# Kernel tuning notes

Measured on AMD Instinct MI355X. Metric: run time of the kernel, lower is better.

Reference implementation:

```python
import jax, jax.numpy as jnp
import numpy as np

EPS = 1e-5
DN = ('NCHW', 'OIHW', 'NCHW')


def _conv3x3(x, w):
    return jax.lax.conv_general_dilated(x, w, (1, 1), 'SAME', dimension_numbers=DN)


def _bn_relu(x, g, b):
    # eval-mode BN: running_mean=0, running_var=1
    scale = (g / jnp.sqrt(1.0 + EPS))[None, :, None, None]
    return jax.nn.relu(x * scale + b[None, :, None, None])


def _double_conv(x, w1, g1, b1, w2, g2, b2):
    x = _bn_relu(_conv3x3(x, w1), g1, b1)
    return _bn_relu(_conv3x3(x, w2), g2, b2)


def _up2x_bilinear_align(x):
    # bilinear, align_corners=True, scale_factor=2
    def interp(a, axis, n_in):
        n_out = 2 * n_in
        pos = jnp.arange(n_out, dtype=jnp.float32) * (n_in - 1) / (n_out - 1)
        lo = jnp.floor(pos).astype(jnp.int32)
        hi = jnp.minimum(lo + 1, n_in - 1)
        w = pos - lo.astype(jnp.float32)
        sh = [1, 1, 1, 1]
        sh[axis] = n_out
        w = w.reshape(sh)
        return jnp.take(a, lo, axis=axis) * (1.0 - w) + jnp.take(a, hi, axis=axis) * w
    B, C, H, W = x.shape
    return interp(interp(x, 2, H), 3, W)


def _lstm_dir(seq, Wih, Whh, bih, bhh, reverse):
    # seq: (N, T, C) -> (N, T, Hh); PyTorch gate order i,f,g,o
    Hh = Whh.shape[1]
    xg = jnp.einsum('ntc,gc->ntg', seq, Wih) + (bih + bhh)
    if reverse:
        xg = xg[:, ::-1]
    xg = jnp.swapaxes(xg, 0, 1)  # (T, N, 4H)
    N = seq.shape[0]
    h0 = jnp.zeros((N, Hh), seq.dtype)

    def step(carry, gx):
        h, c = carry
        g = gx + h @ Whh.T
        i, f, gg, o = jnp.split(g, 4, axis=-1)
        c = jax.nn.sigmoid(f) * c + jax.nn.sigmoid(i) * jnp.tanh(gg)
        h = jax.nn.sigmoid(o) * jnp.tanh(c)
        return (h, c), h

    _, hs = jax.lax.scan(step, (h0, h0), xg)
    hs = jnp.swapaxes(hs, 0, 1)  # (N, T, Hh)
    if reverse:
        hs = hs[:, ::-1]
    return hs


def _bilstm(seq, Wf, Uf, bif, bhf, Wb, Ub, bib, bhb):
    return jnp.concatenate([
        _lstm_dir(seq, Wf, Uf, bif, bhf, False),
        _lstm_dir(seq, Wb, Ub, bib, bhb, True),
    ], axis=-1)


def _site_rows(x, lstm):
    # batched version of per-row LSTM: each row is a sequence over W, features C
    B, C, H, W = x.shape
    s = jnp.transpose(x, (0, 2, 3, 1)).reshape(B * H, W, C)
    out = _bilstm(s, *lstm)  # (B*H, W, C) since 2*hidden == C
    return jnp.transpose(out.reshape(B, H, W, C), (0, 3, 1, 2))


def _site_cols(x, lstm):
    # each column is a sequence over H, features C
    B, C, H, W = x.shape
    s = jnp.transpose(x, (0, 3, 2, 1)).reshape(B * W, H, C)
    out = _bilstm(s, *lstm)
    return jnp.transpose(out.reshape(B, W, H, C), (0, 3, 2, 1))


def setup_inputs() -> dict:
    key = jax.random.key(0)
    ks = jax.random.split(key, 24)
    d = {}
    d['x1'] = jax.random.normal(ks[0], (8, 128, 32, 32), jnp.float32)
    d['x2'] = jax.random.normal(ks[1], (8, 128, 64, 64), jnp.float32)
    # bidirectional LSTM: input 256, hidden 128
    d['lstm_Wih_f'] = jax.random.normal(ks[2], (512, 256), jnp.float32) * 0.06
    d['lstm_Whh_f'] = jax.random.normal(ks[3], (512, 128), jnp.float32) * 0.08
    d['lstm_bih_f'] = jax.random.normal(ks[4], (512,), jnp.float32) * 0.05
    d['lstm_bhh_f'] = jax.random.normal(ks[5], (512,), jnp.float32) * 0.05
    d['lstm_Wih_b'] = jax.random.normal(ks[6], (512, 256), jnp.float32) * 0.06
    d['lstm_Whh_b'] = jax.random.normal(ks[7], (512, 128), jnp.float32) * 0.08
    d['lstm_bib_tmp'] = None
    del d['lstm_bib_tmp']
    d['lstm_bih_b'] = jax.random.normal(ks[8], (512,), jnp.float32) * 0.05
    d['lstm_bhh_b'] = jax.random.normal(ks[9], (512,), jnp.float32) * 0.05
    # conv_2 = DoubleConv(512, 256) (mid=256), shared across its two call sites
    d['c2_w1'] = jax.random.normal(ks[10], (256, 512, 3, 3), jnp.float32) * 0.02
    d['c2_g1'] = jax.random.uniform(ks[11], (256,), jnp.float32, 0.5, 1.5)
    d['c2_b1'] = jax.random.normal(ks[12], (256,), jnp.float32) * 0.05
    d['c2_w2'] = jax.random.normal(ks[13], (256, 256, 3, 3), jnp.float32) * 0.03
    d['c2_g2'] = jax.random.uniform(ks[14], (256,), jnp.float32, 0.5, 1.5)
    d['c2_b2'] = jax.random.normal(ks[15], (256,), jnp.float32) * 0.05
    # conv = DoubleConv(256, 128, mid=128)
    d['cv_w1'] = jax.random.normal(ks[16], (128, 256, 3, 3), jnp.float32) * 0.03
    d['cv_g1'] = jax.random.uniform(ks[17], (128,), jnp.float32, 0.5, 1.5)
    d['cv_b1'] = jax.random.normal(ks[18], (128,), jnp.float32) * 0.05
    d['cv_w2'] = jax.random.normal(ks[19], (128, 128, 3, 3), jnp.float32) * 0.04
    d['cv_g2'] = jax.random.uniform(ks[20], (128,), jnp.float32, 0.5, 1.5)
    d['cv_b2'] = jax.random.normal(ks[21], (128,), jnp.float32) * 0.05
    return d


def reference(x1, x2, lstm_Wih_f, lstm_Whh_f, lstm_bih_f, lstm_bhh_f,
              lstm_Wih_b, lstm_Whh_b, lstm_bih_b, lstm_bhh_b,
              c2_w1, c2_g1, c2_b1, c2_w2, c2_g2, c2_b2,
              cv_w1, cv_g1, cv_b1, cv_w2, cv_g2, cv_b2):
    lstm = (lstm_Wih_f, lstm_Whh_f, lstm_bih_f, lstm_bhh_f,
            lstm_Wih_b, lstm_Whh_b, lstm_bih_b, lstm_bhh_b)
    x1u = _up2x_bilinear_align(x1)
    dy = x2.shape[2] - x1u.shape[2]
    dx = x2.shape[3] - x1u.shape[3]
    x1u = jnp.pad(x1u, ((0, 0), (0, 0), (dy // 2, dy - dy // 2), (dx // 2, dx - dx // 2)))
    x = jnp.concatenate([x2, x1u], axis=1)  # (B, 256, 64, 64)
    # site_relation mutates x in-place in torch: rows pass, then cols pass on the
    # row-updated tensor; x_weigth and x_heigth alias the same final tensor.
    x = _site_rows(x, lstm)
    x = _site_cols(x, lstm)
    x_site = jnp.concatenate([x, x], axis=1)  # (B, 512, H, W)
    x_site = _double_conv(x_site, c2_w1, c2_g1, c2_b1, c2_w2, c2_g2, c2_b2)
    x = jnp.concatenate([x, x_site], axis=1)  # (B, 512, H, W)
    x = _double_conv(x, c2_w1, c2_g1, c2_b1, c2_w2, c2_g2, c2_b2)
    x = _double_conv(x, cv_w1, cv_g1, cv_b1, cv_w2, cv_g2, cv_b2)
    return x  # (B, 128, 64, 64)
```

## Files before the change

kernel.cpp:

```cpp
#include <hip/hip_runtime.h>
#include <hip/hip_bf16.h>
#include <math.h>

typedef __bf16 bf16x8 __attribute__((ext_vector_type(8)));
typedef float  f32x4  __attribute__((ext_vector_type(4)));

__device__ __forceinline__ float sigm(float x) {
  return __builtin_amdgcn_rcpf(1.f + __expf(-x));
}
__device__ __forceinline__ float tanh_f(float x) {
  return 2.f*__builtin_amdgcn_rcpf(1.f + __expf(-2.f*x)) - 1.f;
}
__device__ __forceinline__ float b2f(unsigned short u){
  unsigned int x = ((unsigned int)u) << 16; return __uint_as_float(x);
}
__device__ __forceinline__ unsigned short f2b(float v){
  __hip_bfloat16 h = __float2bfloat16(v); return *(unsigned short*)&h;
}
__device__ __forceinline__ void glds16(const void* g, void* l) {
  __builtin_amdgcn_global_load_lds(
      (const __attribute__((address_space(1))) unsigned int*)g,
      (__attribute__((address_space(3))) unsigned int*)l, 16, 0, 0);
}
__device__ __forceinline__ bf16x8 bzero() {
  bf16x8 v;
  #pragma unroll
  for (int i = 0; i < 8; ++i) v[i] = (__bf16)0.0f;
  return v;
}
__device__ __forceinline__ void barrier_lds() {
  asm volatile("s_waitcnt lgkmcnt(0)\n\ts_barrier" ::: "memory");
}

__global__ __launch_bounds__(256) void k_upcat(const float* __restrict__ x1,
                                               const float* __restrict__ x2,
                                               __hip_bfloat16* __restrict__ X0) {
  int idx = blockIdx.x*256 + threadIdx.x;
  int c = idx & 255;
  int w = (idx >> 8) & 63;
  int h = (idx >> 14) & 63;
  int n = idx >> 20;
  float v;
  if (c < 128) {
    v = x2[((n*128 + c)*64 + h)*64 + w];
  } else {
    int cc = c - 128;
    float py = (h*31.0f)/63.0f;
    int ly = (int)py; int hy = min(ly+1, 31); float fy = py - (float)ly;
    float px = (w*31.0f)/63.0f;
    int lx = (int)px; int hx = min(lx+1, 31); float fx = px - (float)lx;
    const float* p = x1 + (size_t)(n*128 + cc)*1024;
    float v00 = p[ly*32+lx], v01 = p[ly*32+hx];
    float v10 = p[hy*32+lx], v11 = p[hy*32+hx];
    v = (1.f-fy)*((1.f-fx)*v00 + fx*v01) + fy*((1.f-fx)*v10 + fx*v11);
  }
  X0[idx] = __float2bfloat16(v);
}

__global__ __launch_bounds__(256) void k_wih_prep(
    const float* __restrict__ Wf, const float* __restrict__ Wb,
    const float* __restrict__ bif, const float* __restrict__ bhf,
    const float* __restrict__ bib, const float* __restrict__ bhb,
    __hip_bfloat16* __restrict__ wihc, float* __restrict__ biasc) {
  int idx = blockIdx.x*256 + threadIdx.x;
  int n = idx >> 8, k = idx & 255;
  float v = (n < 512) ? Wf[n*256 + k] : Wb[(n-512)*256 + k];
  wihc[idx] = __float2bfloat16(v);
  if (idx < 1024) biasc[idx] = (idx < 512) ? bif[idx] + bhf[idx]
                                           : bib[idx-512] + bhb[idx-512];
}

__global__ __launch_bounds__(256) void k_xg_gemm(
    const __hip_bfloat16* __restrict__ Xin,
    const __hip_bfloat16* __restrict__ Wihc,
    const float* __restrict__ biasc,
    __hip_bfloat16* __restrict__ xg) {
  __shared__ __align__(16) unsigned short sa[128][72];
  __shared__ __align__(16) unsigned short sw[128][72];
  int bx = blockIdx.x;
  int t = bx >> 2, seq0 = (bx & 3) << 7;
  int n0 = blockIdx.y << 7;
  int tid = threadIdx.x, lane = tid & 63, wid = tid >> 6;
  int wm = wid >> 1, wn = wid & 1;
  int l15 = lane & 15, quad = lane >> 4;
  f32x4 acc[4][4];
  #pragma unroll
  for (int i = 0; i < 4; ++i)
    #pragma unroll
    for (int j = 0; j < 4; ++j) acc[i][j] = (f32x4){0.f,0.f,0.f,0.f};

  for (int k0 = 0; k0 < 256; k0 += 64) {
    __syncthreads();
    for (int idx = tid; idx < 2048; idx += 256) {
      int row = idx >> 4, c4 = (idx & 15) << 2;
      *(ushort4*)&sa[row][c4] = *(const ushort4*)((const unsigned short*)Xin +
          (size_t)((seq0 + row)*64 + t)*256 + k0 + c4);
      *(ushort4*)&sw[row][c4] = *(const ushort4*)((const unsigned short*)Wihc +
          (size_t)(n0 + row)*256 + k0 + c4);
    }
    __syncthreads();
    #pragma unroll
    for (int k32 = 0; k32 < 64; k32 += 32) {
      bf16x8 af[4], bfr[4];
      #pragma unroll
      for (int mt = 0; mt < 4; ++mt)
        af[mt] = *(const bf16x8*)&sa[wm*64 + mt*16 + l15][k32 + quad*8];
      #pragma unroll
      for (int nt = 0; nt < 4; ++nt)
        bfr[nt] = *(const bf16x8*)&sw[wn*64 + nt*16 + l15][k32 + quad*8];
      #pragma unroll
      for (int mt = 0; mt < 4; ++mt)
        #pragma unroll
        for (int nt = 0; nt < 4; ++nt)
          acc[mt][nt] = __builtin_amdgcn_mfma_f32_16x16x32_bf16(
              af[mt], bfr[nt], acc[mt][nt], 0, 0, 0);
    }
  }
  #pragma unroll
  for (int nt = 0; nt < 4; ++nt) {
    int cg = n0 + wn*64 + nt*16 + l15;
    int dir = cg >> 9;
    int g   = (cg >> 7) & 3;
    int u   = cg & 127;
    float bias = biasc[cg];
    unsigned short* op = (unsigned short*)xg +
        (size_t)(((dir*64 + t)*4 + g)*512)*128 + u;
    #pragma unroll
    for (int mt = 0; mt < 4; ++mt) {
      int sbase = seq0 + wm*64 + mt*16 + quad*4;
      f32x4 a = acc[mt][nt];
      #pragma unroll
      for (int r = 0; r < 4; ++r)
        op[(size_t)(sbase + r)*128] = f2b(a[r] + bias);
    }
  }
}

__global__ __launch_bounds__(256, 1) void k_lstm_rec(
    const __hip_bfloat16* __restrict__ xg,
    const float* __restrict__ WhhF, const float* __restrict__ WhhB,
    __hip_bfloat16* __restrict__ out) {
  const int dir = blockIdx.y;
  const int sb  = blockIdx.x;
  const float* Whh = dir ? WhhB : WhhF;
  __shared__ __align__(16) unsigned short hs[16][136];
  __shared__ __align__(16) float gv[4][128][4];
  const int tid = threadIdx.x, lane = tid & 63, wv = tid >> 6;
  const int l15 = lane & 15, quad = lane >> 4;

  bf16x8 wf[4][2][4];
  #pragma unroll
  for (int g = 0; g < 4; ++g)
    #pragma unroll
    for (int ut = 0; ut < 2; ++ut) {
      int gate = g*128 + wv*32 + ut*16 + l15;
      #pragma unroll
      for (int kc = 0; kc < 4; ++kc) {
        const float* wp = Whh + (size_t)gate*128 + kc*32 + quad*8;
        float4 w0 = *(const float4*)wp;
        float4 w1 = *(const float4*)(wp + 4);
        bf16x8 f;
        f[0]=(__bf16)w0.x; f[1]=(__bf16)w0.y; f[2]=(__bf16)w0.z; f[3]=(__bf16)w0.w;
        f[4]=(__bf16)w1.x; f[5]=(__bf16)w1.y; f[6]=(__bf16)w1.z; f[7]=(__bf16)w1.w;
        wf[g][ut][kc] = f;
      }
    }
  for (int i = tid; i < 16*136; i += 256) ((unsigned short*)hs)[i] = 0;

  const int u_  = tid & 127;
  const int s0_ = tid >> 7;
  float cst[2] = {0.f, 0.f};

  const unsigned short* xp = (const unsigned short*)xg +
      (size_t)dir*64*4*512*128;
  unsigned short xv[2][4], xn[2][4];
  #define LDX(stp, dst)                                                    \
    {                                                                      \
      int ts_ = (stp) < 64 ? (stp) : 63;                                   \
      int t_  = dir ? 63 - ts_ : ts_;                                      \
      _Pragma("unroll")                                                    \
      for (int j_ = 0; j_ < 2; ++j_) {                                     \
        int s_ = s0_ + j_*2;                                               \
        _Pragma("unroll")                                                  \
        for (int g_ = 0; g_ < 4; ++g_)                                     \
          dst[j_][g_] = xp[(size_t)((t_*4 + g_)*512 + sb*4 + s_)*128 + u_];\
      }                                                                    \
    }
  LDX(0, xv);
  __syncthreads();

  for (int step = 0; step < 64; ++step) {
    int t = dir ? 63 - step : step;
    LDX(step + 1, xn);
    bf16x8 af[4];
    #pragma unroll
    for (int kc = 0; kc < 4; ++kc)
      af[kc] = *(const bf16x8*)&hs[l15][kc*32 + quad*8];
    f32x4 acc[4][2];
    #pragma unroll
    for (int g = 0; g < 4; ++g)
      #pragma unroll
      for (int ut = 0; ut < 2; ++ut) acc[g][ut] = (f32x4){0.f,0.f,0.f,0.f};
    #pragma unroll
    for (int kc = 0; kc < 4; ++kc)
      #pragma unroll
      for (int g = 0; g < 4; ++g)
        #pragma unroll
        for (int ut = 0; ut < 2; ++ut)
          acc[g][ut] = __builtin_amdgcn_mfma_f32_16x16x32_bf16(
              af[kc], wf[g][ut][kc], acc[g][ut], 0, 0, 0);
    if (quad == 0) {
      #pragma unroll
      for (int ut = 0; ut < 2; ++ut) {
        int u = wv*32 + ut*16 + l15;
        #pragma unroll
        for (int r = 0; r < 4; ++r) {
          float4 q;
          q.x = acc[0][ut][r]; q.y = acc[1][ut][r];
          q.z = acc[2][ut][r]; q.w = acc[3][ut][r];
          *(float4*)&gv[r][u][0] = q;
        }
      }
    }
    barrier_lds();
    #pragma unroll
    for (int j = 0; j < 2; ++j) {
      int s = s0_ + j*2;
      float4 gq = *(const float4*)&gv[s][u_][0];
      float I = gq.x + b2f(xv[j][0]);
      float F = gq.y + b2f(xv[j][1]);
      float G = gq.z + b2f(xv[j][2]);
      float O = gq.w + b2f(xv[j][3]);
      float cv = sigm(F)*cst[j] + sigm(I)*tanh_f(G);
      float hv = sigm(O)*tanh_f(cv);
      cst[j] = cv;
      unsigned short hb = f2b(hv);
      hs[s][u_] = hb;
      int gs = sb*4 + s;
      ((unsigned short*)out)[(size_t)(((gs >> 6)*64 + t)*64 + (gs & 63))*256
                             + dir*128 + u_] = hb;
    }
    barrier_lds();
    #pragma unroll
    for (int j = 0; j < 2; ++j)
      #pragma unroll
      for (int g = 0; g < 4; ++g) xv[j][g] = xn[j][g];
  }
  #undef LDX
}

__global__ __launch_bounds__(256) void k_wrefmt_bf16(const float* __restrict__ src,
                                                     __hip_bfloat16* __restrict__ dst,
                                                     int Ci, int Co, int fold) {
  int idx = blockIdx.x*256 + threadIdx.x;
  int total = 9*Ci*Co;
  if (idx >= total) return;
  int ci = idx % Ci;
  int co = (idx / Ci) % Co;
  int k  = idx / (Ci*Co);
  int CiS = fold ? Ci*2 : Ci;
  float v = src[(size_t)(co*CiS + ci)*9 + k];
  if (fold) v += src[(size_t)(co*CiS + ci + Ci)*9 + k];
  dst[idx] = __float2bfloat16(v);
}

__global__ __launch_bounds__(256, 2) void k_conv3_v3(
    const __hip_bfloat16* __restrict__ inA, const __hip_bfloat16* __restrict__ inB,
    const __hip_bfloat16* __restrict__ wgt,
    const float* __restrict__ gam, const float* __restrict__ bet,
    float* __restrict__ outF, __hip_bfloat16* __restrict__ outB,
    int Cin, int Co, int nchw) {
  __shared__ __align__(16) unsigned short si[6][64][64];
  __shared__ __align__(16) unsigned short sw[3][64][64];
  int bx = blockIdx.x;
  int n  = bx >> 4;
  int h0 = (bx & 15) << 2;
  int co0 = blockIdx.y << 6;
  int tid = threadIdx.x;
  int lane = tid & 63;
  int wvid = tid >> 6;
  int l15 = lane & 15, quad = lane >> 4;
  int pl = lane >> 3, pc = lane & 7;

  f32x4 acc[4][4];
  #pragma unroll
  for (int i = 0; i < 4; ++i)
    #pragma unroll
    for (int j = 0; j < 4; ++j) acc[i][j] = (f32x4){0.f,0.f,0.f,0.f};

  int cs = inB ? 256 : Cin;
  for (int ci0 = 0; ci0 < Cin; ci0 += 64) {
    const unsigned short* src = (const unsigned short*)inA; int cb = ci0;
    if (inB && ci0 >= 256) { src = (const unsigned short*)inB; cb = ci0 - 256; }
    __syncthreads();
    #pragma unroll
    for (int j = 0; j < 12; ++j) {
      int s = wvid + j*4;
      int row = s >> 3, grp = s & 7;
      int ih = h0 + row - 1;
      if (ih >= 0 && ih <= 63) {
        const unsigned short* gsrc = src + (size_t)((n*64 + ih)*64)*cs + cb;
        int iw = grp*8 + pl;
        int lc = pc ^ (iw & 7);
        glds16(gsrc + (size_t)iw*cs + lc*8, &si[row][grp*8][0]);
      } else {
        uint4 z = {0,0,0,0};
        *(uint4*)((unsigned short*)&si[row][grp*8][0] + lane*8) = z;
      }
    }
    for (int ky = 0; ky < 3; ++ky) {
      if (ky) __syncthreads();
      {
        const unsigned short* wk = (const unsigned short*)wgt +
            (size_t)(ky*3*Co + co0)*Cin + ci0;
        #pragma unroll
        for (int j = 0; j < 6; ++j) {
          int s = wvid + j*4;
          int kx = s >> 3, cg = s & 7;
          int co = cg*8 + pl;
          int lc = pc ^ (co & 7);
          glds16(wk + (size_t)(kx*Co + co)*Cin + lc*8, &sw[kx][cg*8][0]);
        }
      }
      __syncthreads();
      int row = wvid + ky;
      #pragma unroll
      for (int kx = 0; kx < 3; ++kx) {
        #pragma unroll
        for (int k32 = 0; k32 < 2; ++k32) {
          bf16x8 af[4], bfr[4];
          #pragma unroll
          for (int mt = 0; mt < 4; ++mt) {
            int iw = mt*16 + l15 + kx - 1;
            int iwc = iw & 63;
            int pcc = (k32*4 + quad) ^ (iwc & 7);
            af[mt] = *(const bf16x8*)&si[row][iwc][pcc*8];
            if ((kx == 0 && mt == 0 && l15 == 0) ||
                (kx == 2 && mt == 3 && l15 == 15))
              af[mt] = bzero();
          }
          #pragma unroll
          for (int nt = 0; nt < 4; ++nt) {
            int co = nt*16 + l15;
            int pcc = (k32*4 + quad) ^ (co & 7);
            bfr[nt] = *(const bf16x8*)&sw[kx][co][pcc*8];
          }
          #pragma unroll
          for (int mt = 0; mt < 4; ++mt)
            #pragma unroll
            for (int nt = 0; nt < 4; ++nt)
              acc[mt][nt] = __builtin_amdgcn_mfma_f32_16x16x32_bf16(
                  af[mt], bfr[nt], acc[mt][nt], 0, 0, 0);
        }
      }
    }
  }
  const float kS = 0.9999950000374997f;
  int h = h0 + wvid;
  #pragma unroll
  for (int nt = 0; nt < 4; ++nt) {
    int co = co0 + nt*16 + l15;
    float scale = gam[co]*kS, bb = bet[co];
    #pragma unroll
    for (int mt = 0; mt < 4; ++mt) {
      f32x4 a = acc[mt][nt];
      #pragma unroll
      for (int r = 0; r < 4; ++r) {
        int w = mt*16 + quad*4 + r;
        float v = fmaf(a[r], scale, bb);
        v = v > 0.f ? v : 0.f;
        if (nchw) outF[(size_t)((n*Co + co)*64 + h)*64 + w] = v;
        else      outB[(size_t)((n*64 + h)*64 + w)*Co + co] = __float2bfloat16(v);
      }
    }
  }
}

extern "C" void kernel_launch(void* const* d_in, const int* in_sizes, int n_in,
                              void* d_out, int out_size, void* d_ws, size_t ws_size,
                              hipStream_t stream) {
  const float* x1    = (const float*)d_in[0];
  const float* x2    = (const float*)d_in[1];
  const float* Wih_f = (const float*)d_in[2];
  const float* Whh_f = (const float*)d_in[3];
  const float* bih_f = (const float*)d_in[4];
  const float* bhh_f = (const float*)d_in[5];
  const float* Wih_b = (const float*)d_in[6];
  const float* Whh_b = (const float*)d_in[7];
  const float* bih_b = (const float*)d_in[8];
  const float* bhh_b = (const float*)d_in[9];
  const float* c2_w1 = (const float*)d_in[10];
  const float* c2_g1 = (const float*)d_in[11];
  const float* c2_b1 = (const float*)d_in[12];
  const float* c2_w2 = (const float*)d_in[13];
  const float* c2_g2 = (const float*)d_in[14];
  const float* c2_b2 = (const float*)d_in[15];
  const float* cv_w1 = (const float*)d_in[16];
  const float* cv_g1 = (const float*)d_in[17];
  const float* cv_b1 = (const float*)d_in[18];
  const float* cv_w2 = (const float*)d_in[19];
  const float* cv_g2 = (const float*)d_in[20];
  const float* cv_b2 = (const float*)d_in[21];

  char* base = (char*)d_ws;
  const size_t SLOTB = 16777216ull;
  __hip_bfloat16* Xb  = (__hip_bfloat16*)(base);
  __hip_bfloat16* Sb  = (__hip_bfloat16*)(base);
  __hip_bfloat16* XG  = (__hip_bfloat16*)(base + SLOTB);
  __hip_bfloat16* D2  = (__hip_bfloat16*)(base + SLOTB);
  __hip_bfloat16* D2b = (__hip_bfloat16*)(base + 2*SLOTB);
  __hip_bfloat16* RT  = (__hip_bfloat16*)(base + SLOTB + 67108864ull);
  __hip_bfloat16* D1  = RT;
  char* wq = base + SLOTB + 67108864ull + SLOTB;
  __hip_bfloat16* wihc  = (__hip_bfloat16*)wq;
  float*          biasc = (float*)(wq + 524288);
  char* cw = wq + 528384;
  __hip_bfloat16* w1f    = (__hip_bfloat16*)(cw);
  __hip_bfloat16* w1full = (__hip_bfloat16*)(cw + 1179648);
  __hip_bfloat16* w2r    = (__hip_bfloat16*)(cw + 3538944);
  __hip_bfloat16* wv1    = (__hip_bfloat16*)(cw + 4718592);
  __hip_bfloat16* wv2    = (__hip_bfloat16*)(cw + 5308416);

  k_wih_prep<<<1024, 256, 0, stream>>>(Wih_f, Wih_b, bih_f, bhh_f, bih_b, bhh_b,
                                       wihc, biasc);
  k_wrefmt_bf16<<<(9*256*256+255)/256, 256, 0, stream>>>(c2_w1, w1f,    256, 256, 1);
  k_wrefmt_bf16<<<(9*512*256+255)/256, 256, 0, stream>>>(c2_w1, w1full, 512, 256, 0);
  k_wrefmt_bf16<<<(9*256*256+255)/256, 256, 0, stream>>>(c2_w2, w2r,    256, 256, 0);
  k_wrefmt_bf16<<<(9*256*128+255)/256, 256, 0, stream>>>(cv_w1, wv1,    256, 128, 0);
  k_wrefmt_bf16<<<(9*128*128+255)/256, 256, 0, stream>>>(cv_w2, wv2,    128, 128, 0);

  k_upcat<<<32768, 256, 0, stream>>>(x1, x2, Xb);

  k_xg_gemm<<<dim3(256, 8), 256, 0, stream>>>(Xb, wihc, biasc, XG);
  k_lstm_rec<<<dim3(128, 2), 256, 0, stream>>>(XG, Whh_f, Whh_b, RT);
  k_xg_gemm<<<dim3(256, 8), 256, 0, stream>>>(RT, wihc, biasc, XG);
  k_lstm_rec<<<dim3(128, 2), 256, 0, stream>>>(XG, Whh_f, Whh_b, Sb);

  k_conv3_v3<<<dim3(128,4), 256, 0, stream>>>(Sb, nullptr, w1f, c2_g1, c2_b1,
                                              nullptr, D1, 256, 256, 0);
  k_conv3_v3<<<dim3(128,4), 256, 0, stream>>>(D1, nullptr, w2r, c2_g2, c2_b2,
                                              nullptr, D2, 256, 256, 0);
  k_conv3_v3<<<dim3(128,4), 256, 0, stream>>>(Sb, D2, w1full, c2_g1, c2_b1,
                                              nullptr, D2b, 512, 256, 0);
  k_conv3_v3<<<dim3(128,4), 256, 0, stream>>>(D2b, nullptr, w2r, c2_g2, c2_b2,
                                              nullptr, D1, 256, 256, 0);
  k_conv3_v3<<<dim3(128,2), 256, 0, stream>>>(D1, nullptr, wv1, cv_g1, cv_b1,
                                              nullptr, D2, 256, 128, 0);
  k_conv3_v3<<<dim3(128,2), 256, 0, stream>>>(D2, nullptr, wv2, cv_g2, cv_b2,
                                              (float*)d_out, nullptr, 128, 128, 1);
}
```

Baseline: 632.1 us.

## Compute LSTM gates in MFMA registers and double-buffer hidden state

The LSTM recurrent kernel now runs the gate nonlinearities directly on the MFMA accumulator registers. Each lane selects its own row from the accumulator instead of staging gate values through an LDS buffer. The hidden state is double-buffered in LDS, so each timestep needs one barrier instead of two. This shortens the serial per-step critical path, at the cost of all four quads doing redundant MFMA rows and selecting values with extra conditional moves.

```diff
diff --git a/kernel.cpp b/kernel.cpp
--- a/kernel.cpp
+++ b/kernel.cpp
@@ -143,8 +143,7 @@
   const int dir = blockIdx.y;
   const int sb  = blockIdx.x;
   const float* Whh = dir ? WhhB : WhhF;
-  __shared__ __align__(16) unsigned short hs[16][136];
-  __shared__ __align__(16) float gv[4][128][4];
+  __shared__ __align__(16) unsigned short hs[2][4][136];
   const int tid = threadIdx.x, lane = tid & 63, wv = tid >> 6;
   const int l15 = lane & 15, quad = lane >> 4;
 
@@ -165,37 +164,42 @@
         wf[g][ut][kc] = f;
       }
     }
-  for (int i = tid; i < 16*136; i += 256) ((unsigned short*)hs)[i] = 0;
-
-  const int u_  = tid & 127;
-  const int s0_ = tid >> 7;
+  for (int i = tid; i < 2*4*136; i += 256) ((unsigned short*)hs)[i] = 0;
+
   float cst[2] = {0.f, 0.f};
 
   const unsigned short* xp = (const unsigned short*)xg +
       (size_t)dir*64*4*512*128;
   unsigned short xv[2][4], xn[2][4];
-  #define LDX(stp, dst)                                                    \
-    {                                                                      \
-      int ts_ = (stp) < 64 ? (stp) : 63;                                   \
-      int t_  = dir ? 63 - ts_ : ts_;                                      \
-      _Pragma("unroll")                                                    \
-      for (int j_ = 0; j_ < 2; ++j_) {                                     \
-        int s_ = s0_ + j_*2;                                               \
-        _Pragma("unroll")                                                  \
-        for (int g_ = 0; g_ < 4; ++g_)                                     \
-          dst[j_][g_] = xp[(size_t)((t_*4 + g_)*512 + sb*4 + s_)*128 + u_];\
-      }                                                                    \
+  #define LDX(stp, dst)                                                     \
+    {                                                                       \
+      int ts_ = (stp) < 64 ? (stp) : 63;                                    \
+      int t_  = dir ? 63 - ts_ : ts_;                                       \
+      _Pragma("unroll")                                                     \
+      for (int ut_ = 0; ut_ < 2; ++ut_) {                                   \
+        _Pragma("unroll")                                                   \
+        for (int g_ = 0; g_ < 4; ++g_)                                      \
+          dst[ut_][g_] = xp[(size_t)((t_*4 + g_)*512 + sb*4 + quad)*128     \
+                            + wv*32 + ut_*16 + l15];                        \
+      }                                                                     \
     }
   LDX(0, xv);
   __syncthreads();
+
+  const int gs = sb*4 + quad;
+  unsigned short* outb = (unsigned short*)out +
+      (size_t)(gs >> 6)*64*64*256 + (size_t)(gs & 63)*256 + dir*128;
+  const bool qa = (quad & 1) != 0;
+  const bool qb = (quad & 2) != 0;
 
   for (int step = 0; step < 64; ++step) {
     int t = dir ? 63 - step : step;
     LDX(step + 1, xn);
+    const int cur = step & 1;
     bf16x8 af[4];
     #pragma unroll
     for (int kc = 0; kc < 4; ++kc)
-      af[kc] = *(const bf16x8*)&hs[l15][kc*32 + quad*8];
+      af[kc] = *(const bf16x8*)&hs[cur][l15 & 3][kc*32 + quad*8];
     f32x4 acc[4][2];
     #pragma unroll
     for (int g = 0; g < 4; ++g)
@@ -209,42 +213,33 @@
         for (int ut = 0; ut < 2; ++ut)
           acc[g][ut] = __builtin_amdgcn_mfma_f32_16x16x32_bf16(
               af[kc], wf[g][ut][kc], acc[g][ut], 0, 0, 0);
-    if (quad == 0) {
-      #pragma unroll
-      for (int ut = 0; ut < 2; ++ut) {
-        int u = wv*32 + ut*16 + l15;
-        #pragma unroll
-        for (int r = 0; r < 4; ++r) {
-          float4 q;
-          q.x = acc[0][ut][r]; q.y = acc[1][ut][r];
-          q.z = acc[2][ut][r]; q.w = acc[3][ut][r];
-          *(float4*)&gv[r][u][0] = q;
-        }
-      }
+    #pragma unroll
+    for (int ut = 0; ut < 2; ++ut) {
+      float gsel[4];
+      #pragma unroll
+      for (int g = 0; g < 4; ++g) {
+        f32x4 a = acc[g][ut];
+        float v01 = qa ? a[1] : a[0];
+        float v23 = qa ? a[3] : a[2];
+        gsel[g] = qb ? v23 : v01;
+      }
+      float I = gsel[0] + b2f(xv[ut][0]);
+      float F = gsel[1] + b2f(xv[ut][1]);
+      float G = gsel[2] + b2f(xv[ut][2]);
+      float O = gsel[3] + b2f(xv[ut][3]);
+      float cv = sigm(F)*cst[ut] + sigm(I)*tanh_f(G);
+      float hv = sigm(O)*tanh_f(cv);
+      cst[ut] = cv;
+      unsigned short hb = f2b(hv);
+      int u = wv*32 + ut*16 + l15;
+      hs[cur ^ 1][quad][u] = hb;
+      outb[(size_t)t*16384 + u] = hb;
     }
     barrier_lds();
     #pragma unroll
-    for (int j = 0; j < 2; ++j) {
-      int s = s0_ + j*2;
-      float4 gq = *(const float4*)&gv[s][u_][0];
-      float I = gq.x + b2f(xv[j][0]);
-      float F = gq.y + b2f(xv[j][1]);
-      float G = gq.z + b2f(xv[j][2]);
-      float O = gq.w + b2f(xv[j][3]);
-      float cv = sigm(F)*cst[j] + sigm(I)*tanh_f(G);
-      float hv = sigm(O)*tanh_f(cv);
-      cst[j] = cv;
-      unsigned short hb = f2b(hv);
-      hs[s][u_] = hb;
-      int gs = sb*4 + s;
-      ((unsigned short*)out)[(size_t)(((gs >> 6)*64 + t)*64 + (gs & 63))*256
-                             + dir*128 + u_] = hb;
-    }
-    barrier_lds();
-    #pragma unroll
-    for (int j = 0; j < 2; ++j)
-      #pragma unroll
-      for (int g = 0; g < 4; ++g) xv[j][g] = xn[j][g];
+    for (int ut = 0; ut < 2; ++ut)
+      #pragma unroll
+      for (int g = 0; g < 4; ++g) xv[ut][g] = xn[ut][g];
   }
   #undef LDX
 }
```

Measured after the change: 613.1 us. 1.03x faster.
